# Optimization experiments

Hardware: AMD Instinct MI355X
Metric: run time of the kernel (lower is better)

The kernel has to match this reference:

```python
import jax, jax.numpy as jnp
import numpy as np
from jax import lax

# program token ids
PAD, START, END, SCENE, INTERSECT, FILT, RELATE, QUERY = range(8)
SKIP = (PAD, START, END)


def conv2d(x, w, b, dil=1):
    # 'same' padding for odd kernels (3x3 pad=dil, 1x1 pad=0), NCHW/OIHW
    pad = dil * (w.shape[2] // 2)
    y = lax.conv_general_dilated(x, w, (1, 1), [(pad, pad), (pad, pad)],
                                 rhs_dilation=(dil, dil),
                                 dimension_numbers=('NCHW', 'OIHW', 'NCHW'))
    return y + b[None, :, None, None]


def maxpool2(x):
    return lax.reduce_window(x, -jnp.inf, lax.max, (1, 1, 2, 2), (1, 1, 2, 2), 'VALID')


def exec_program(prog, feat_input, p):
    """Run one (concrete) program over a batch of stem features. prog: tuple of ints,
    executed in reversed order exactly like TbDNet.forward."""
    B, _, H, W = feat_input.shape
    output = feat_input
    saved = None
    for t in reversed(prog):
        if t in SKIP:
            continue
        if t == SCENE:
            saved = output
            output = jnp.ones((B, 1, H, W), feat_input.dtype)
        elif t == INTERSECT:  # AndModule: elementwise min of attentions
            output = jnp.minimum(output, saved)
        elif t == FILT:
            a = feat_input * output  # [B,D,H,W] * [B,1,H,W]
            a = jax.nn.relu(conv2d(a, p['att_w1'], p['att_b1']))
            a = jax.nn.relu(conv2d(a, p['att_w2'], p['att_b2']))
            output = jax.nn.sigmoid(conv2d(a, p['att_w3'], p['att_b3']))
        elif t == RELATE:  # RelateModule: dilated conv stack (1,2,4,8,1) -> conv1x1 sigmoid
            a = feat_input * output
            for w, b, d in ((p['rel_w1'], p['rel_b1'], 1), (p['rel_w2'], p['rel_b2'], 2),
                            (p['rel_w3'], p['rel_b3'], 4), (p['rel_w4'], p['rel_b4'], 8),
                            (p['rel_w5'], p['rel_b5'], 1)):
                a = jax.nn.relu(conv2d(a, w, b, d))
            output = jax.nn.sigmoid(conv2d(a, p['rel_w6'], p['rel_b6']))
        elif t == QUERY:
            a = feat_input * output
            a = jax.nn.relu(conv2d(a, p['qry_w1'], p['qry_b1']))
            output = jax.nn.relu(conv2d(a, p['qry_w2'], p['qry_b2']))
    return output


def tbd_forward(feats, programs_np, p):
    B = feats.shape[0]
    stem = jax.nn.relu(conv2d(feats, p['stem_w1'], p['stem_b1']))
    stem = jax.nn.relu(conv2d(stem, p['stem_w2'], p['stem_b2']))  # [B,D,H,W]
    D, H, W = stem.shape[1], stem.shape[2], stem.shape[3]
    # group samples by identical program so dispatch runs batched, not per-sample
    groups = {}
    for n in range(B):
        groups.setdefault(tuple(int(v) for v in programs_np[n]), []).append(n)
    mod_out = jnp.zeros((B, D, H, W), feats.dtype)
    for prog, idxs in groups.items():
        idx = jnp.array(idxs)
        mod_out = mod_out.at[idx].set(exec_program(prog, stem[idx], p))
    # classifier: conv1x1 -> relu -> maxpool2 -> flatten -> fc -> relu -> fc
    x = jax.nn.relu(conv2d(mod_out, p['cls_w'], p['cls_b']))
    x = maxpool2(x)                        # [B,1024,7,7]
    x = x.reshape(B, -1)                   # [B,50176]
    x = jax.nn.relu(x @ p['fc1_w'].T + p['fc1_b'])
    return x @ p['fc2_w'].T + p['fc2_b']   # [B,28]


def setup_inputs() -> dict:
    key = jax.random.key(0)
    ks = iter(jax.random.split(key, 64))
    def rn(shape, s=0.05):
        return jax.random.normal(next(ks), shape, dtype=jnp.float32) * s
    B, Cin, H, W, D, P, L, A = 64, 1024, 14, 14, 128, 1024, 1024, 28
    feats = jax.random.normal(next(ks), (B, Cin, H, W), dtype=jnp.float32)
    # stored programs; execution order is reversed(stored)
    progA = [START, QUERY, FILT, RELATE, FILT, SCENE, END, PAD]            # scene->filter->relate->filter->query
    progB = [START, QUERY, INTERSECT, FILT, SCENE, FILT, SCENE, END]       # two filter branches -> intersect -> query
    programs = jnp.array([progA] * (B // 2) + [progB] * (B // 2), dtype=jnp.int32)
    inp = {'feats': feats, 'programs': programs,
           'stem_w1': rn((D, Cin, 3, 3), 0.02), 'stem_b1': rn((D,)),
           'stem_w2': rn((D, D, 3, 3)), 'stem_b2': rn((D,)),
           'att_w1': rn((D, D, 3, 3)), 'att_b1': rn((D,)),
           'att_w2': rn((D, D, 3, 3)), 'att_b2': rn((D,)),
           'att_w3': rn((1, D, 1, 1)), 'att_b3': rn((1,)),
           'rel_w1': rn((D, D, 3, 3)), 'rel_b1': rn((D,)),
           'rel_w2': rn((D, D, 3, 3)), 'rel_b2': rn((D,)),
           'rel_w3': rn((D, D, 3, 3)), 'rel_b3': rn((D,)),
           'rel_w4': rn((D, D, 3, 3)), 'rel_b4': rn((D,)),
           'rel_w5': rn((D, D, 3, 3)), 'rel_b5': rn((D,)),
           'rel_w6': rn((1, D, 1, 1)), 'rel_b6': rn((1,)),
           'qry_w1': rn((D, D, 3, 3)), 'qry_b1': rn((D,)),
           'qry_w2': rn((D, D, 3, 3)), 'qry_b2': rn((D,)),
           'cls_w': rn((P, D, 1, 1)), 'cls_b': rn((P,)),
           'fc1_w': rn((L, P * (H // 2) * (W // 2)), 0.01), 'fc1_b': rn((L,)),
           'fc2_w': rn((A, L)), 'fc2_b': rn((A,))}
    return inp


PARAM_NAMES = ['stem_w1', 'stem_b1', 'stem_w2', 'stem_b2',
               'att_w1', 'att_b1', 'att_w2', 'att_b2', 'att_w3', 'att_b3',
               'rel_w1', 'rel_b1', 'rel_w2', 'rel_b2', 'rel_w3', 'rel_b3',
               'rel_w4', 'rel_b4', 'rel_w5', 'rel_b5', 'rel_w6', 'rel_b6',
               'qry_w1', 'qry_b1', 'qry_w2', 'qry_b2',
               'cls_w', 'cls_b', 'fc1_w', 'fc1_b', 'fc2_w', 'fc2_b']


def reference(feats, programs, stem_w1, stem_b1, stem_w2, stem_b2,
              att_w1, att_b1, att_w2, att_b2, att_w3, att_b3,
              rel_w1, rel_b1, rel_w2, rel_b2, rel_w3, rel_b3,
              rel_w4, rel_b4, rel_w5, rel_b5, rel_w6, rel_b6,
              qry_w1, qry_b1, qry_w2, qry_b2,
              cls_w, cls_b, fc1_w, fc1_b, fc2_w, fc2_b):
    vals = [stem_w1, stem_b1, stem_w2, stem_b2,
            att_w1, att_b1, att_w2, att_b2, att_w3, att_b3,
            rel_w1, rel_b1, rel_w2, rel_b2, rel_w3, rel_b3,
            rel_w4, rel_b4, rel_w5, rel_b5, rel_w6, rel_b6,
            qry_w1, qry_b1, qry_w2, qry_b2,
            cls_w, cls_b, fc1_w, fc1_b, fc2_w, fc2_b]
    p = dict(zip(PARAM_NAMES, vals))
    return tbd_forward(feats, np.asarray(programs), p)
```

## Files before the change

kernel.cpp:

```cpp
#include <hip/hip_runtime.h>
#include <math.h>


typedef __attribute__((ext_vector_type(8)))  short   short8;
typedef __attribute__((ext_vector_type(8)))  __bf16  bf16x8;
typedef __attribute__((ext_vector_type(4)))  float   f32x4;

#define NROUNDS 11
#define NKS 98

#define B_WSTEM1 0UL
#define B_WSTEM2 2359296UL
#define B_WMOD   2654208UL
#define B_WCLS   5308416UL
#define B_STEM   5570560UL
#define B_XA     8781824UL
#define B_XB     11993088UL
#define B_FEAT   15204352UL
#define B_ATTN   18415616UL
#define B_SAVED  18465792UL
#define B_SCHED  18515968UL
#define B_ACTB   18520064UL
#define B_FC1T   24942592UL
#define B_P1X1   25204736UL
#define B_S1P    67108864UL
#define B_FC1P   100663296UL

__device__ __forceinline__ unsigned short f2bf(float f) {
    unsigned int b = __float_as_uint(f);
    b += 0x7fffu + ((b >> 16) & 1u);
    return (unsigned short)(b >> 16);
}
__device__ __forceinline__ float bf2f(unsigned short u) {
    return __uint_as_float(((unsigned int)u) << 16);
}
__device__ __forceinline__ f32x4 mfma16(bf16x8 a, bf16x8 b, f32x4 c) {
    return __builtin_amdgcn_mfma_f32_16x16x32_bf16(a, b, c, 0, 0, 0);
}

struct PrepArgs { const float* src[12]; const int* prog; char* ws; };

__global__ __launch_bounds__(256) void k_prep(PrepArgs a)
{
    char* ws = a.ws;
    const int bx = blockIdx.x;
    if (bx < 768) {
        const int y = bx >> 6;
        const float* __restrict__ src = a.src[y];
        int gid = (bx & 63) * 256 + threadIdx.x;
        int gsz = 64 * 256;
        if (y == 11) {
            unsigned short* dst = (unsigned short*)(ws + B_WCLS);
            for (int i = gid; i < 131072; i += gsz) dst[i] = f2bf(src[i]);
        } else {
            const int IC = (y == 0) ? 1024 : 128;
            const int lg = (y == 0) ? 10 : 7;
            unsigned short* dst = (unsigned short*)(ws + ((y == 0) ? B_WSTEM1
                                        : (y == 1) ? B_WSTEM2
                                        : B_WMOD + (size_t)(y - 2) * 294912));
            const int total = 9 << (lg + 7);
            for (int i = gid; i < total; i += gsz) {
                int ic = i & (IC - 1);
                int oc = (i >> lg) & 127;
                int t  = i >> (lg + 7);
                dst[i] = f2bf(src[((size_t)oc * IC + ic) * 9 + t]);
            }
        }
        return;
    }
    int gid = (bx - 768) * 256 + threadIdx.x;
    int gsz = 256 * 256;
    float* attn  = (float*)(ws + B_ATTN);
    float* saved = (float*)(ws + B_SAVED);
    float* p1    = (float*)(ws + B_P1X1);
    for (int i = gid; i < 64 * 196; i += gsz) { attn[i] = 1.0f; saved[i] = 1.0f; }
    for (int i = gid; i < 8 * 64 * 196; i += gsz) p1[i] = 0.0f;
    unsigned int* fz = (unsigned int*)(ws + B_FEAT);
    for (int i = gid; i < 64 * 25088 / 2; i += gsz) fz[i] = 0u;
    if (gid < 64) {
        int n = gid;
        const int* prog = a.prog;
        int ent[NROUNDS];
        for (int r = 0; r < NROUNDS; ++r) ent[r] = 0;
        int rc = 0, nslot = 0;
        int pscene = 0, pinter = 0, pmat = 0, pmw = 0;
#define PREBITS ((pscene<<17)|(pinter<<18)|(pmat<<19)|(pmw<<22))
#define CLRPRE  (pscene = pinter = pmat = pmw = 0)
#define EMIT(v) do { if (rc < NROUNDS) ent[rc++] = (v); } while (0)
        for (int j = 7; j >= 0; --j) {
            int t = prog[n * 8 + j];
            switch (t) {
                case 3: pscene = 1; break;
                case 4: pinter = 1; break;
                case 5: {
                    int e1 = 3 | (0<<4) | (1<<8) | (1<<12) | (2<<13) | (0<<15) | PREBITS;
                    CLRPRE; EMIT(e1);
                    EMIT(3 | (1<<4) | (1<<8) | (0<<12) | (0<<13) | (1<<15)
                           | (1<<23) | (0<<24) | (nslot<<25));
                    pmat = nslot + 1; pmw = 0; nslot++;
                    break;
                }
                case 6: {
                    int e1 = 3 | (2<<4) | (1<<8) | (1<<12) | (2<<13) | (0<<15) | PREBITS;
                    CLRPRE; EMIT(e1);
                    EMIT(3 | (3<<4) | (2<<8) | (0<<12) | (0<<13) | (1<<15));
                    EMIT(3 | (4<<4) | (4<<8) | (0<<12) | (1<<13) | (0<<15));
                    EMIT(3 | (5<<4) | (8<<8) | (0<<12) | (0<<13) | (1<<15));
                    EMIT(3 | (6<<4) | (1<<8) | (0<<12) | (1<<13) | (0<<15)
                           | (1<<23) | (1<<24) | (nslot<<25));
                    pmat = nslot + 1; pmw = 1; nslot++;
                    break;
                }
                case 7: {
                    int e1 = 3 | (7<<4) | (1<<8) | (1<<12) | (2<<13) | (0<<15) | PREBITS;
                    CLRPRE; EMIT(e1);
                    EMIT(3 | (8<<4) | (1<<8) | (0<<12) | (0<<13) | (2<<15));
                    break;
                }
                default: break;
            }
        }
#undef EMIT
#undef PREBITS
#undef CLRPRE
        int* sched = (int*)(ws + B_SCHED);
        for (int r = 0; r < NROUNDS; ++r) sched[n * NROUNDS + r] = ent[r];
    }
}

__global__ __launch_bounds__(512) void k_stem1p(const float* __restrict__ feats,
                                                const unsigned short* __restrict__ wrep,
                                                char* ws)
{
    __shared__ unsigned short s_img[197 * 136];
    const int bx = blockIdx.x;
    const int n = bx >> 3, ks = bx & 7;
    const int tid = threadIdx.x, lane = tid & 63;
    const int w = tid >> 6, wm = w & 1, wn = w >> 1;
    const int l15 = lane & 15, lq = lane >> 4;

    if (tid < 68) ((unsigned int*)s_img)[196 * 68 + tid] = 0u;

    int pglob[4], pbyt[4], pyv[4], pxv[4];
#pragma unroll
    for (int j = 0; j < 4; ++j) {
        int p  = (wn + 4 * j) * 16 + l15;
        pglob[j] = p;
        int py = p / 14;
        pyv[j] = (p < 196) ? py : 10000;
        pxv[j] = p - py * 14;
        pbyt[j] = p * 272 + lq * 16;
    }
    const int zaddr = 196 * 272 + lq * 16;
    const int nJ = (wn == 0) ? 4 : 3;

    f32x4 acc[4][4];
#pragma unroll
    for (int m = 0; m < 4; ++m)
#pragma unroll
        for (int j = 0; j < 4; ++j) acc[m][j] = (f32x4){0.f, 0.f, 0.f, 0.f};

    const int icg = tid & 31;
    const int qq0 = tid >> 5;
    const int icb = ks * 128;

    const float* sf = feats + ((size_t)n * 1024 + icb) * 196;
    for (int qq = qq0; qq < 49; qq += 16) {
        const float* p0 = sf + icg * 4 * 196 + qq * 4;
        float4 r0 = *(const float4*)(p0);
        float4 r1 = *(const float4*)(p0 + 196);
        float4 r2 = *(const float4*)(p0 + 392);
        float4 r3 = *(const float4*)(p0 + 588);
#pragma unroll
        for (int e = 0; e < 4; ++e) {
            uint2 v;
            v.x = (unsigned int)f2bf(((const float*)&r0)[e]) |
                  ((unsigned int)f2bf(((const float*)&r1)[e]) << 16);
            v.y = (unsigned int)f2bf(((const float*)&r2)[e]) |
                  ((unsigned int)f2bf(((const float*)&r3)[e]) << 16);
            *(uint2*)(s_img + (qq * 4 + e) * 136 + icg * 4) = v;
        }
    }
    __syncthreads();

#pragma unroll
    for (int t = 0; t < 9; ++t) {
        const int dy = t / 3 - 1, dx = t % 3 - 1;
        int baddr[4];
#pragma unroll
        for (int j = 0; j < 4; ++j) {
            int yy = pyv[j] + dy, xx = pxv[j] + dx;
            bool ok = ((unsigned)yy < 14u) && ((unsigned)xx < 14u);
            baddr[j] = ok ? (pbyt[j] + (dy * 14 + dx) * 272) : zaddr;
        }
#pragma unroll
        for (int kc = 0; kc < 4; ++kc) {
            const unsigned short* wt = wrep +
                ((size_t)(t * 128 + wm * 64 + l15) * 1024 + icb + kc * 32 + lq * 8);
            bf16x8 am[4];
#pragma unroll
            for (int m = 0; m < 4; ++m)
                am[m] = *(const bf16x8*)(wt + (size_t)m * 16 * 1024);
#pragma unroll
            for (int j = 0; j < 4; ++j) {
                if (j < nJ) {
                    bf16x8 b = *(const bf16x8*)((const char*)s_img + baddr[j] + kc * 64);
#pragma unroll
                    for (int m = 0; m < 4; ++m)
                        acc[m][j] = mfma16(am[m], b, acc[m][j]);
                }
            }
        }
    }

    unsigned short* part = (unsigned short*)(ws + B_S1P);
#pragma unroll
    for (int m = 0; m < 4; ++m) {
        const int oc = wm * 64 + m * 16 + lq * 4;
#pragma unroll
        for (int j = 0; j < 4; ++j) {
            if (j < nJ) {
                int p = pglob[j];
                if (p < 196) {
                    unsigned int lo = (unsigned int)f2bf(acc[m][j][0]) |
                                      ((unsigned int)f2bf(acc[m][j][1]) << 16);
                    unsigned int hi = (unsigned int)f2bf(acc[m][j][2]) |
                                      ((unsigned int)f2bf(acc[m][j][3]) << 16);
                    uint2 pk; pk.x = lo; pk.y = hi;
                    *(uint2*)(part + (((size_t)ks * 64 + n) * 196 + p) * 128 + oc) = pk;
                }
            }
        }
    }
}

__global__ __launch_bounds__(256) void k_stem1r(const char* __restrict__ ws_c,
                                                const float* __restrict__ bias,
                                                unsigned short* __restrict__ xa)
{
    int i = blockIdx.x * 256 + threadIdx.x;
    const unsigned short* part = (const unsigned short*)(ws_c + B_S1P);
    int oc8 = (i & 15) * 8;
    int np  = i >> 4;
    float s[8] = {};
#pragma unroll
    for (int ks = 0; ks < 8; ++ks) {
        short8 v = *(const short8*)(part + (((size_t)ks * 64) * 196 + np) * 128 + oc8);
#pragma unroll
        for (int e = 0; e < 8; ++e) s[e] += bf2f((unsigned short)v[e]);
    }
    short8 o;
#pragma unroll
    for (int e = 0; e < 8; ++e)
        o[e] = (short)f2bf(fmaxf(s[e] + bias[oc8 + e], 0.f));
    *(short8*)(xa + (size_t)np * 128 + oc8) = o;
}

__device__ void conv_core32(const unsigned short* __restrict__ srcB,
                            const float* __restrict__ s_gate,
                            const unsigned short* __restrict__ wrep,
                            const float* __restrict__ bias,
                            unsigned short* __restrict__ dst,
                            int dil, int oct, int pxh,
                            unsigned short* s_img,
                            int post, const float* __restrict__ pwv,
                            float* __restrict__ pdst)
{
    const int tid  = threadIdx.x, lane = tid & 63;
    const int w    = tid >> 6, wm = w & 1, wn = w >> 1;
    const int l15  = lane & 15, lq = lane >> 4;

    if (tid < 68) ((unsigned int*)s_img)[196 * 68 + tid] = 0u;

    int pglob[4], pbyt[4], pyv[4], pxv[4];
#pragma unroll
    for (int j = 0; j < 4; ++j) {
        int nt = wn + 2 * j;
        int p  = (pxh * 7 + nt) * 16 + l15;
        pglob[j] = p;
        int py = p / 14;
        pyv[j] = (p < 196) ? py : 10000;
        pxv[j] = p - py * 14;
        pbyt[j] = p * 272 + lq * 16;
    }
    const int zaddr = 196 * 272 + lq * 16;
    const int nNT = (wn == 0) ? 4 : 3;

    f32x4 acc[4];
#pragma unroll
    for (int j = 0; j < 4; ++j) acc[j] = (f32x4){0.f, 0.f, 0.f, 0.f};

    if (s_gate) {
        for (int i = tid; i < 196 * 16; i += 256) {
            int p = i >> 4, c8 = (i & 15) * 8;
            short8 v = *(const short8*)(srcB + p * 128 + c8);
            float g = s_gate[p];
            short8 ov;
#pragma unroll
            for (int e = 0; e < 8; ++e)
                ov[e] = (short)f2bf(bf2f((unsigned short)v[e]) * g);
            *(short8*)(s_img + p * 136 + c8) = ov;
        }
    } else {
        for (int i = tid; i < 196 * 16; i += 256) {
            int p = i >> 4, c8 = (i & 15) * 8;
            *(short8*)(s_img + p * 136 + c8) = *(const short8*)(srcB + p * 128 + c8);
        }
    }
    __syncthreads();

    const unsigned short* wlane = wrep + (size_t)(oct * 32 + wm * 16 + l15) * 128 + lq * 8;
#pragma unroll
    for (int t = 0; t < 9; ++t) {
        const int dy = (t / 3 - 1) * dil, dx = (t % 3 - 1) * dil;
        int baddr[4];
#pragma unroll
        for (int j = 0; j < 4; ++j) {
            int yy = pyv[j] + dy, xx = pxv[j] + dx;
            bool ok = ((unsigned)yy < 14u) && ((unsigned)xx < 14u);
            baddr[j] = ok ? (pbyt[j] + (dy * 14 + dx) * 272) : zaddr;
        }
        const unsigned short* wt = wlane + (size_t)(t * 128) * 128;
#pragma unroll
        for (int kc = 0; kc < 4; ++kc) {
            bf16x8 a0 = *(const bf16x8*)(wt + kc * 32);
#pragma unroll
            for (int j = 0; j < 4; ++j) {
                if (j < nNT) {
                    bf16x8 b = *(const bf16x8*)((const char*)s_img + baddr[j] + kc * 64);
                    acc[j] = mfma16(a0, b, acc[j]);
                }
            }
        }
    }

    const int oc = oct * 32 + wm * 16 + lq * 4;
    const float4 b4 = *(const float4*)(bias + oc);
    float4 wv4;
    if (post) wv4 = *(const float4*)(pwv + oc);
#pragma unroll
    for (int j = 0; j < 4; ++j) {
        if (j < nNT) {
            int p = pglob[j];
            if (p < 196) {
                float v0 = fmaxf(acc[j][0] + b4.x, 0.f);
                float v1 = fmaxf(acc[j][1] + b4.y, 0.f);
                float v2 = fmaxf(acc[j][2] + b4.z, 0.f);
                float v3 = fmaxf(acc[j][3] + b4.w, 0.f);
                uint2 pk;
                pk.x = (unsigned int)f2bf(v0) | ((unsigned int)f2bf(v1) << 16);
                pk.y = (unsigned int)f2bf(v2) | ((unsigned int)f2bf(v3) << 16);
                *(uint2*)(dst + p * 128 + oc) = pk;
                if (post) {
                    float s = v0 * wv4.x + v1 * wv4.y + v2 * wv4.z + v3 * wv4.w;
                    atomicAdd(pdst + p, s);
                }
            }
        }
    }
}

__global__ __launch_bounds__(256) void k_conv_stem2(const unsigned short* __restrict__ srcBall,
                                                    const unsigned short* __restrict__ wrep,
                                                    const float* __restrict__ bias,
                                                    unsigned short* __restrict__ dstall)
{
    __shared__ unsigned short s_img[197 * 136];
    const int n = blockIdx.x >> 3, oct = (blockIdx.x >> 1) & 3, pxh = blockIdx.x & 1;
    conv_core32(srcBall + (size_t)n * 25088, nullptr, wrep, bias,
                dstall + (size_t)n * 25088, 1, oct, pxh, s_img, 0, nullptr, nullptr);
}

struct RArgs {
    char* ws;
    const float* mbias[9];
    const float* w1x1[2];
    const float* b1x1[2];
};

__global__ __launch_bounds__(256) void k_round(RArgs a, int r)
{
    __shared__ unsigned short s_img[197 * 136];
    __shared__ float s_gate[196];
    const int bx = blockIdx.x;
    const int n = bx >> 3, oct = (bx >> 1) & 3, pxh = bx & 1;
    char* ws = a.ws;
    const int* sched = (const int*)(ws + B_SCHED);
    const int e = sched[n * NROUNDS + r];
    if ((e & 15) == 0) return;
    const int tid = threadIdx.x;
    const int wset = (e >> 4) & 15, dil = (e >> 8) & 15, gatef = (e >> 12) & 1;
    const int srcid = (e >> 13) & 3, dstid = (e >> 15) & 3;
    const int fscene = (e >> 17) & 1, finter = (e >> 18) & 1;
    const int mslot = (e >> 19) & 7, mw = (e >> 22) & 1;
    const int post = (e >> 23) & 1, pw = (e >> 24) & 1, pslot = (e >> 25) & 7;

    float* attn  = (float*)(ws + B_ATTN)  + n * 196;
    float* saved = (float*)(ws + B_SAVED) + n * 196;
    float* p1    = (float*)(ws + B_P1X1);

    if (gatef) {
        if (tid < 196) {
            float cur = attn[tid];
            if (mslot) {
                float pv = p1[(size_t)(mslot - 1) * 12544 + n * 196 + tid];
                cur = 1.0f / (1.0f + __expf(-(pv + a.b1x1[mw][0])));
            }
            if (fscene) { saved[tid] = cur; cur = 1.0f; }
            if (finter) { cur = fminf(cur, saved[tid]); }
            if (mslot | fscene | finter) attn[tid] = cur;
            s_gate[tid] = cur;
        }
        __syncthreads();
    }

    const unsigned short* src = (const unsigned short*)(ws +
            (srcid == 2 ? B_STEM : srcid == 1 ? B_XB : B_XA)) + (size_t)n * 25088;
    unsigned short* dst = (unsigned short*)(ws +
            (dstid == 2 ? B_FEAT : dstid == 1 ? B_XB : B_XA)) + (size_t)n * 25088;
    const unsigned short* wrep = (const unsigned short*)(ws + B_WMOD) + (size_t)wset * 9 * 128 * 128;

    conv_core32(src, gatef ? s_gate : nullptr, wrep, a.mbias[wset], dst,
                dil, oct, pxh, s_img,
                post, post ? a.w1x1[pw] : nullptr,
                post ? (p1 + (size_t)pslot * 12544 + n * 196) : nullptr);
}

__global__ __launch_bounds__(256) void k_cls_pool(const unsigned short* __restrict__ featall,
                                                  const unsigned short* __restrict__ clsw,
                                                  const float* __restrict__ clsb,
                                                  unsigned short* __restrict__ actB)
{
    __shared__ char smem[197 * 272 + 64 * 200 * 4];
    unsigned short* s_img = (unsigned short*)smem;
    float* s_pool = (float*)(smem + 197 * 272);
    const int n = blockIdx.x >> 4, pt = blockIdx.x & 15;
    const int tid = threadIdx.x, lane = tid & 63, w = tid >> 6;
    const int l15 = lane & 15, lq = lane >> 4;
    const unsigned short* feat = featall + (size_t)n * 25088;

    if (tid < 68) ((unsigned int*)s_img)[196 * 68 + tid] = 0u;
    for (int i = tid; i < 196 * 16; i += 256) {
        int p = i >> 4, c8 = (i & 15) * 8;
        *(short8*)(s_img + p * 136 + c8) = *(const short8*)(feat + p * 128 + c8);
    }
    f32x4 acc[14];
#pragma unroll
    for (int j = 0; j < 14; ++j) acc[j] = (f32x4){0.f, 0.f, 0.f, 0.f};
    __syncthreads();

    const unsigned short* wl = clsw + (size_t)(pt * 64 + w * 16 + l15) * 128 + lq * 8;
#pragma unroll
    for (int kc = 0; kc < 4; ++kc) {
        bf16x8 a0 = *(const bf16x8*)(wl + kc * 32);
#pragma unroll
        for (int j = 0; j < 14; ++j) {
            int p = j * 16 + l15;
            int ba = (p < 196) ? (p * 272 + lq * 16 + kc * 64) : (196 * 272 + lq * 16);
            bf16x8 b = *(const bf16x8*)((const char*)s_img + ba);
            acc[j] = mfma16(a0, b, acc[j]);
        }
    }
    const int oc = pt * 64 + w * 16 + lq * 4;
    const float4 b4 = *(const float4*)(clsb + oc);
    const int pl = w * 16 + lq * 4;
#pragma unroll
    for (int j = 0; j < 14; ++j) {
        int p = j * 16 + l15;
        if (p < 196) {
            s_pool[(pl + 0) * 200 + p] = fmaxf(acc[j][0] + b4.x, 0.f);
            s_pool[(pl + 1) * 200 + p] = fmaxf(acc[j][1] + b4.y, 0.f);
            s_pool[(pl + 2) * 200 + p] = fmaxf(acc[j][2] + b4.z, 0.f);
            s_pool[(pl + 3) * 200 + p] = fmaxf(acc[j][3] + b4.w, 0.f);
        }
    }
    __syncthreads();
    for (int i = tid; i < 64 * 49; i += 256) {
        int plx = i / 49, q = i - plx * 49;
        int py = q / 7, qx = q - py * 7;
        const float* rp = s_pool + plx * 200 + py * 28 + qx * 2;
        float m = fmaxf(fmaxf(rp[0], rp[1]), fmaxf(rp[14], rp[15]));
        int k = (pt * 64 + plx) * 49 + q;
        int kb = k >> 6, lq2 = (k >> 4) & 3, hi = (k >> 3) & 1, e = k & 7;
        actB[((((size_t)kb * 4 + lq2) * 2 + hi) * 64 + n) * 8 + e] = f2bf(m);
    }
}

__global__ __launch_bounds__(256) void k_fc1p(const unsigned short* __restrict__ actB,
                                              const float* __restrict__ w,
                                              float* __restrict__ part)
{
    __shared__ float s_w[64 * 128];
    const int jt = blockIdx.x & 15, ks = blockIdx.x >> 4;
    const int tid = threadIdx.x, lane = tid & 63, wv = tid >> 6;
    const int l15 = lane & 15, lq = lane >> 4;
    const int k0 = ks * 512;

    f32x4 acc[4];
#pragma unroll
    for (int t = 0; t < 4; ++t) acc[t] = (f32x4){0.f, 0.f, 0.f, 0.f};

    const int half  = lane >> 5;
    const int chunk = lane & 31;
    const int srow  = wv * 16 + l15;
    const int ssw   = srow & 7;
    const float* arow = s_w + srow * 128;
    const float* wbase = w + (size_t)(jt * 64) * 50176 + k0;

    for (int st = 0; st < 4; ++st) {
        __syncthreads();
#pragma unroll
        for (int i = 0; i < 8; ++i) {
            const int r0 = wv * 16 + i * 2;
            const int rr = r0 + half;
            const int g  = chunk ^ (rr & 7);
            const float* src = wbase + (size_t)rr * 50176 + st * 128 + g * 4;
            __builtin_amdgcn_global_load_lds(
                (const __attribute__((address_space(1))) unsigned int*)src,
                (__attribute__((address_space(3))) unsigned int*)(s_w + r0 * 128),
                16, 0, 0);
        }
        __syncthreads();

        const int kbase = k0 + st * 128;
#pragma unroll
        for (int kk = 0; kk < 4; ++kk) {
            const int u0 = kk * 8 + lq * 2;
            float4 f0 = *(const float4*)(arow + ((u0 ^ ssw) << 2));
            float4 f1 = *(const float4*)(arow + (((u0 + 1) ^ ssw) << 2));
            bf16x8 a;
            a[0] = (__bf16)f0.x; a[1] = (__bf16)f0.y; a[2] = (__bf16)f0.z; a[3] = (__bf16)f0.w;
            a[4] = (__bf16)f1.x; a[5] = (__bf16)f1.y; a[6] = (__bf16)f1.z; a[7] = (__bf16)f1.w;
            const int kglob = kbase + kk * 32 + lq * 8;
            const int kb = kglob >> 6, lq2 = (kglob >> 4) & 3, hi = (kglob >> 3) & 1;
            const unsigned short* bp = actB +
                ((((size_t)kb * 4 + lq2) * 2 + hi) * 64 + l15) * 8;
#pragma unroll
            for (int t = 0; t < 4; ++t) {
                bf16x8 b = *(const bf16x8*)(bp + t * 128);
                acc[t] = mfma16(a, b, acc[t]);
            }
        }
    }

    float* pbase = part + ((size_t)ks * 1024 + jt * 64 + wv * 16 + lq * 4) * 64 + l15;
#pragma unroll
    for (int t = 0; t < 4; ++t)
#pragma unroll
        for (int r = 0; r < 4; ++r)
            pbase[(size_t)r * 64 + t * 16] = acc[t][r];
}

__global__ __launch_bounds__(256) void k_fc1r(const float* __restrict__ part,
                                              const float* __restrict__ b,
                                              float* __restrict__ fc1T)
{
    int i = blockIdx.x * 256 + threadIdx.x;
    if (i >= 65536) return;
    float s = 0.0f;
    for (int ks = 0; ks < NKS; ++ks) s += part[(size_t)ks * 65536 + i];
    int j = i >> 6;
    fc1T[i] = fmaxf(s + b[j], 0.0f);
}

__global__ __launch_bounds__(256) void k_fc2(const float* __restrict__ fc1T,
                                             const float* __restrict__ w,
                                             const float* __restrict__ b,
                                             float* __restrict__ out)
{
    __shared__ float red[256];
    const int a_ = blockIdx.x;
    const int tid = threadIdx.x, lane = tid & 63, q = tid >> 6;
    float acc = 0.0f;
    const float* wr = w + (size_t)a_ * 1024;
    for (int k = q * 256; k < q * 256 + 256; ++k)
        acc = fmaf(fc1T[k * 64 + lane], wr[k], acc);
    red[tid] = acc;
    __syncthreads();
    if (q == 0) {
        float s = red[tid] + red[tid + 64] + red[tid + 128] + red[tid + 192] + b[a_];
        out[lane * 28 + a_] = s;
    }
}

extern "C" void kernel_launch(void* const* d_in, const int* in_sizes, int n_in,
                              void* d_out, int out_size, void* d_ws, size_t ws_size,
                              hipStream_t stream)
{
    const float* feats = (const float*)d_in[0];
    const int*   prog  = (const int*)d_in[1];
    char* ws  = (char*)d_ws;
    float* out = (float*)d_out;

    PrepArgs pa;
    pa.src[0]  = (const float*)d_in[2];
    pa.src[1]  = (const float*)d_in[4];
    pa.src[2]  = (const float*)d_in[6];
    pa.src[3]  = (const float*)d_in[8];
    pa.src[4]  = (const float*)d_in[12];
    pa.src[5]  = (const float*)d_in[14];
    pa.src[6]  = (const float*)d_in[16];
    pa.src[7]  = (const float*)d_in[18];
    pa.src[8]  = (const float*)d_in[20];
    pa.src[9]  = (const float*)d_in[24];
    pa.src[10] = (const float*)d_in[26];
    pa.src[11] = (const float*)d_in[28];
    pa.prog = prog;
    pa.ws = ws;
    k_prep<<<1024, 256, 0, stream>>>(pa);

    k_stem1p<<<512, 512, 0, stream>>>(feats, (const unsigned short*)(ws + B_WSTEM1), ws);
    k_stem1r<<<784, 256, 0, stream>>>(ws, (const float*)d_in[3],
                                      (unsigned short*)(ws + B_XA));

    k_conv_stem2<<<512, 256, 0, stream>>>((const unsigned short*)(ws + B_XA),
                                          (const unsigned short*)(ws + B_WSTEM2),
                                          (const float*)d_in[5],
                                          (unsigned short*)(ws + B_STEM));

    RArgs ga;
    ga.ws = ws;
    ga.mbias[0] = (const float*)d_in[7];
    ga.mbias[1] = (const float*)d_in[9];
    ga.mbias[2] = (const float*)d_in[13];
    ga.mbias[3] = (const float*)d_in[15];
    ga.mbias[4] = (const float*)d_in[17];
    ga.mbias[5] = (const float*)d_in[19];
    ga.mbias[6] = (const float*)d_in[21];
    ga.mbias[7] = (const float*)d_in[25];
    ga.mbias[8] = (const float*)d_in[27];
    ga.w1x1[0]  = (const float*)d_in[10];
    ga.w1x1[1]  = (const float*)d_in[22];
    ga.b1x1[0]  = (const float*)d_in[11];
    ga.b1x1[1]  = (const float*)d_in[23];

    for (int r = 0; r < NROUNDS; ++r)
        k_round<<<512, 256, 0, stream>>>(ga, r);

    k_cls_pool<<<1024, 256, 0, stream>>>((const unsigned short*)(ws + B_FEAT),
                                         (const unsigned short*)(ws + B_WCLS),
                                         (const float*)d_in[29],
                                         (unsigned short*)(ws + B_ACTB));
    k_fc1p<<<1568, 256, 0, stream>>>((const unsigned short*)(ws + B_ACTB),
                                     (const float*)d_in[30], (float*)(ws + B_FC1P));
    k_fc1r<<<256, 256, 0, stream>>>((const float*)(ws + B_FC1P), (const float*)d_in[31],
                                    (float*)(ws + B_FC1T));
    k_fc2<<<28, 256, 0, stream>>>((const float*)(ws + B_FC1T), (const float*)d_in[32],
                                  (const float*)d_in[33], out);
}
```

Measured before the change: 527.7 us.

## Split stem conv over 16 K-slices and restage fc1 weights as bf16 in LDS

```diff
diff --git a/kernel.cpp b/kernel.cpp
--- a/kernel.cpp
+++ b/kernel.cpp
@@ -8,6 +8,7 @@
 
 #define NROUNDS 11
 #define NKS 98
+#define S1KS 16
 
 #define B_WSTEM1 0UL
 #define B_WSTEM2 2359296UL
@@ -24,15 +25,17 @@
 #define B_FC1T   24942592UL
 #define B_P1X1   25204736UL
 #define B_S1P    67108864UL
-#define B_FC1P   100663296UL
+#define B_FC1P   134217728UL
 
 __device__ __forceinline__ unsigned short f2bf(float f) {
-    unsigned int b = __float_as_uint(f);
-    b += 0x7fffu + ((b >> 16) & 1u);
-    return (unsigned short)(b >> 16);
+    __bf16 h = (__bf16)f;
+    union { __bf16 h; unsigned short u; } c; c.h = h; return c.u;
 }
 __device__ __forceinline__ float bf2f(unsigned short u) {
     return __uint_as_float(((unsigned int)u) << 16);
+}
+__device__ __forceinline__ unsigned int pkbf(float a, float b) {
+    return (unsigned int)f2bf(a) | ((unsigned int)f2bf(b) << 16);
 }
 __device__ __forceinline__ f32x4 mfma16(bf16x8 a, bf16x8 b, f32x4 c) {
     return __builtin_amdgcn_mfma_f32_16x16x32_bf16(a, b, c, 0, 0, 0);
@@ -132,14 +135,14 @@
                                                 const unsigned short* __restrict__ wrep,
                                                 char* ws)
 {
-    __shared__ unsigned short s_img[197 * 136];
+    __shared__ unsigned short s_img[197 * 72];
     const int bx = blockIdx.x;
-    const int n = bx >> 3, ks = bx & 7;
+    const int n = bx >> 4, ks = bx & 15;
     const int tid = threadIdx.x, lane = tid & 63;
     const int w = tid >> 6, wm = w & 1, wn = w >> 1;
     const int l15 = lane & 15, lq = lane >> 4;
 
-    if (tid < 68) ((unsigned int*)s_img)[196 * 68 + tid] = 0u;
+    if (tid < 36) ((unsigned int*)(s_img + 196 * 72))[tid] = 0u;
 
     int pglob[4], pbyt[4], pyv[4], pxv[4];
 #pragma unroll
@@ -149,9 +152,9 @@
         int py = p / 14;
         pyv[j] = (p < 196) ? py : 10000;
         pxv[j] = p - py * 14;
-        pbyt[j] = p * 272 + lq * 16;
-    }
-    const int zaddr = 196 * 272 + lq * 16;
+        pbyt[j] = p * 144 + lq * 16;
+    }
+    const int zaddr = 196 * 144 + lq * 16;
     const int nJ = (wn == 0) ? 4 : 3;
 
     f32x4 acc[4][4];
@@ -160,12 +163,12 @@
 #pragma unroll
         for (int j = 0; j < 4; ++j) acc[m][j] = (f32x4){0.f, 0.f, 0.f, 0.f};
 
-    const int icg = tid & 31;
-    const int qq0 = tid >> 5;
-    const int icb = ks * 128;
+    const int icg = tid & 15;
+    const int qq0 = tid >> 4;
+    const int icb = ks * 64;
 
     const float* sf = feats + ((size_t)n * 1024 + icb) * 196;
-    for (int qq = qq0; qq < 49; qq += 16) {
+    for (int qq = qq0; qq < 49; qq += 32) {
         const float* p0 = sf + icg * 4 * 196 + qq * 4;
         float4 r0 = *(const float4*)(p0);
         float4 r1 = *(const float4*)(p0 + 196);
@@ -174,11 +177,9 @@
 #pragma unroll
         for (int e = 0; e < 4; ++e) {
             uint2 v;
-            v.x = (unsigned int)f2bf(((const float*)&r0)[e]) |
-                  ((unsigned int)f2bf(((const float*)&r1)[e]) << 16);
-            v.y = (unsigned int)f2bf(((const float*)&r2)[e]) |
-                  ((unsigned int)f2bf(((const float*)&r3)[e]) << 16);
-            *(uint2*)(s_img + (qq * 4 + e) * 136 + icg * 4) = v;
+            v.x = pkbf(((const float*)&r0)[e], ((const float*)&r1)[e]);
+            v.y = pkbf(((const float*)&r2)[e], ((const float*)&r3)[e]);
+            *(uint2*)(s_img + (qq * 4 + e) * 72 + icg * 4) = v;
         }
     }
     __syncthreads();
@@ -191,10 +192,10 @@
         for (int j = 0; j < 4; ++j) {
             int yy = pyv[j] + dy, xx = pxv[j] + dx;
             bool ok = ((unsigned)yy < 14u) && ((unsigned)xx < 14u);
-            baddr[j] = ok ? (pbyt[j] + (dy * 14 + dx) * 272) : zaddr;
-        }
-#pragma unroll
-        for (int kc = 0; kc < 4; ++kc) {
+            baddr[j] = ok ? (pbyt[j] + (dy * 14 + dx) * 144) : zaddr;
+        }
+#pragma unroll
+        for (int kc = 0; kc < 2; ++kc) {
             const unsigned short* wt = wrep +
                 ((size_t)(t * 128 + wm * 64 + l15) * 1024 + icb + kc * 32 + lq * 8);
             bf16x8 am[4];
@@ -222,11 +223,9 @@
             if (j < nJ) {
                 int p = pglob[j];
                 if (p < 196) {
-                    unsigned int lo = (unsigned int)f2bf(acc[m][j][0]) |
-                                      ((unsigned int)f2bf(acc[m][j][1]) << 16);
-                    unsigned int hi = (unsigned int)f2bf(acc[m][j][2]) |
-                                      ((unsigned int)f2bf(acc[m][j][3]) << 16);
-                    uint2 pk; pk.x = lo; pk.y = hi;
+                    uint2 pk;
+                    pk.x = pkbf(acc[m][j][0], acc[m][j][1]);
+                    pk.y = pkbf(acc[m][j][2], acc[m][j][3]);
                     *(uint2*)(part + (((size_t)ks * 64 + n) * 196 + p) * 128 + oc) = pk;
                 }
             }
@@ -244,7 +243,7 @@
     int np  = i >> 4;
     float s[8] = {};
 #pragma unroll
-    for (int ks = 0; ks < 8; ++ks) {
+    for (int ks = 0; ks < S1KS; ++ks) {
         short8 v = *(const short8*)(part + (((size_t)ks * 64) * 196 + np) * 128 + oc8);
 #pragma unroll
         for (int e = 0; e < 8; ++e) s[e] += bf2f((unsigned short)v[e]);
@@ -295,11 +294,13 @@
             int p = i >> 4, c8 = (i & 15) * 8;
             short8 v = *(const short8*)(srcB + p * 128 + c8);
             float g = s_gate[p];
-            short8 ov;
-#pragma unroll
-            for (int e = 0; e < 8; ++e)
-                ov[e] = (short)f2bf(bf2f((unsigned short)v[e]) * g);
-            *(short8*)(s_img + p * 136 + c8) = ov;
+            uint2 o0, o1;
+            o0.x = pkbf(bf2f((unsigned short)v[0]) * g, bf2f((unsigned short)v[1]) * g);
+            o0.y = pkbf(bf2f((unsigned short)v[2]) * g, bf2f((unsigned short)v[3]) * g);
+            o1.x = pkbf(bf2f((unsigned short)v[4]) * g, bf2f((unsigned short)v[5]) * g);
+            o1.y = pkbf(bf2f((unsigned short)v[6]) * g, bf2f((unsigned short)v[7]) * g);
+            *(uint2*)(s_img + p * 136 + c8)     = o0;
+            *(uint2*)(s_img + p * 136 + c8 + 4) = o1;
         }
     } else {
         for (int i = tid; i < 196 * 16; i += 256) {
@@ -348,8 +349,8 @@
                 float v2 = fmaxf(acc[j][2] + b4.z, 0.f);
                 float v3 = fmaxf(acc[j][3] + b4.w, 0.f);
                 uint2 pk;
-                pk.x = (unsigned int)f2bf(v0) | ((unsigned int)f2bf(v1) << 16);
-                pk.y = (unsigned int)f2bf(v2) | ((unsigned int)f2bf(v3) << 16);
+                pk.x = pkbf(v0, v1);
+                pk.y = pkbf(v2, v3);
                 *(uint2*)(dst + p * 128 + oc) = pk;
                 if (post) {
                     float s = v0 * wv4.x + v1 * wv4.y + v2 * wv4.z + v3 * wv4.w;
@@ -490,7 +491,7 @@
                                               const float* __restrict__ w,
                                               float* __restrict__ part)
 {
-    __shared__ float s_w[64 * 128];
+    __shared__ unsigned short s_w[64 * 264];
     const int jt = blockIdx.x & 15, ks = blockIdx.x >> 4;
     const int tid = threadIdx.x, lane = tid & 63, wv = tid >> 6;
     const int l15 = lane & 15, lq = lane >> 4;
@@ -500,38 +501,36 @@
 #pragma unroll
     for (int t = 0; t < 4; ++t) acc[t] = (f32x4){0.f, 0.f, 0.f, 0.f};
 
-    const int half  = lane >> 5;
-    const int chunk = lane & 31;
-    const int srow  = wv * 16 + l15;
-    const int ssw   = srow & 7;
-    const float* arow = s_w + srow * 128;
-    const float* wbase = w + (size_t)(jt * 64) * 50176 + k0;
-
-    for (int st = 0; st < 4; ++st) {
+    float4 pf[16];
+
+#define FC1_LOAD(ss_) do {                                                        \
+    _Pragma("unroll")                                                             \
+    for (int pass = 0; pass < 16; ++pass) {                                       \
+        const int row_ = pass * 4 + wv;                                           \
+        pf[pass] = *(const float4*)(w + (size_t)(jt * 64 + row_) * 50176 + k0     \
+                                      + (ss_) * 256 + lane * 4);                  \
+    } } while (0)
+
+    FC1_LOAD(0);
+
+    for (int ss = 0; ss < 2; ++ss) {
         __syncthreads();
 #pragma unroll
-        for (int i = 0; i < 8; ++i) {
-            const int r0 = wv * 16 + i * 2;
-            const int rr = r0 + half;
-            const int g  = chunk ^ (rr & 7);
-            const float* src = wbase + (size_t)rr * 50176 + st * 128 + g * 4;
-            __builtin_amdgcn_global_load_lds(
-                (const __attribute__((address_space(1))) unsigned int*)src,
-                (__attribute__((address_space(3))) unsigned int*)(s_w + r0 * 128),
-                16, 0, 0);
+        for (int pass = 0; pass < 16; ++pass) {
+            const int row = pass * 4 + wv;
+            uint2 v;
+            v.x = pkbf(pf[pass].x, pf[pass].y);
+            v.y = pkbf(pf[pass].z, pf[pass].w);
+            *(uint2*)(s_w + row * 264 + lane * 4) = v;
         }
         __syncthreads();
-
-        const int kbase = k0 + st * 128;
-#pragma unroll
-        for (int kk = 0; kk < 4; ++kk) {
-            const int u0 = kk * 8 + lq * 2;
-            float4 f0 = *(const float4*)(arow + ((u0 ^ ssw) << 2));
-            float4 f1 = *(const float4*)(arow + (((u0 + 1) ^ ssw) << 2));
-            bf16x8 a;
-            a[0] = (__bf16)f0.x; a[1] = (__bf16)f0.y; a[2] = (__bf16)f0.z; a[3] = (__bf16)f0.w;
-            a[4] = (__bf16)f1.x; a[5] = (__bf16)f1.y; a[6] = (__bf16)f1.z; a[7] = (__bf16)f1.w;
-            const int kglob = kbase + kk * 32 + lq * 8;
+        if (ss < 1) FC1_LOAD(1);
+
+        const unsigned short* arow = s_w + (wv * 16 + l15) * 264;
+#pragma unroll
+        for (int kk = 0; kk < 8; ++kk) {
+            bf16x8 a = *(const bf16x8*)(arow + kk * 32 + lq * 8);
+            const int kglob = k0 + ss * 256 + kk * 32 + lq * 8;
             const int kb = kglob >> 6, lq2 = (kglob >> 4) & 3, hi = (kglob >> 3) & 1;
             const unsigned short* bp = actB +
                 ((((size_t)kb * 4 + lq2) * 2 + hi) * 64 + l15) * 8;
@@ -542,6 +541,7 @@
             }
         }
     }
+#undef FC1_LOAD
 
     float* pbase = part + ((size_t)ks * 1024 + jt * 64 + wv * 16 + lq * 4) * 64 + l15;
 #pragma unroll
@@ -609,7 +609,7 @@
     pa.ws = ws;
     k_prep<<<1024, 256, 0, stream>>>(pa);
 
-    k_stem1p<<<512, 512, 0, stream>>>(feats, (const unsigned short*)(ws + B_WSTEM1), ws);
+    k_stem1p<<<1024, 512, 0, stream>>>(feats, (const unsigned short*)(ws + B_WSTEM1), ws);
     k_stem1r<<<784, 256, 0, stream>>>(ws, (const float*)d_in[3],
                                       (unsigned short*)(ws + B_XA));
 
```

Result: faster. 514.7 us (-2.5%).
